# Performance work log

Hardware: AMD Instinct MI355X
Metric: run time of the kernel (lower is better)

Reference implementation:

```python
import jax, jax.numpy as jnp
import numpy as np

IN_DIM = 16384; DM = 512; DEPTH = 4
DI = 1024   # d_inner = expand * d_model
DS = 16     # d_state
DC = 4      # d_conv
DR = 32     # dt_rank = ceil(d_model/16)
B = 4; L = 256


def setup_inputs() -> dict:
    key = jax.random.key(0)
    ks = jax.random.split(key, 12)
    g = lambda k, s, sc=0.02: jax.random.normal(k, s, jnp.float32) * sc
    return {
        "x": jax.random.normal(ks[0], (B, L, IN_DIM), jnp.float32),
        # top-level projections / norm
        "in_w": g(ks[1], (DM, IN_DIM)), "in_b": jnp.zeros((DM,), jnp.float32),
        "ln_g": jnp.ones((DM,), jnp.float32), "ln_b": jnp.zeros((DM,), jnp.float32),
        "out_w": g(ks[2], (IN_DIM, DM)), "out_b": jnp.zeros((IN_DIM,), jnp.float32),
        # stacked per-layer Mamba params (leading dim = DEPTH)
        "m_in_w": g(ks[3], (DEPTH, 2 * DI, DM)),
        "conv_w": g(ks[4], (DEPTH, DI, DC), 0.2),
        "conv_b": jnp.zeros((DEPTH, DI), jnp.float32),
        "xproj_w": g(ks[5], (DEPTH, DR + 2 * DS, DI)),
        "dt_w": g(ks[6], (DEPTH, DI, DR), 0.1),
        "dt_b": jax.random.uniform(ks[7], (DEPTH, DI), jnp.float32, -4.0, -2.0),
        "A_log": jnp.log(jnp.broadcast_to(jnp.arange(1, DS + 1, dtype=jnp.float32), (DEPTH, DI, DS))),
        "D_p": jnp.ones((DEPTH, DI), jnp.float32),
        "m_out_w": g(ks[8], (DEPTH, DM, DI)),
    }


def _mamba(h, iw, cw, cb, xw, dw, db, Alog, Dp, ow):
    """One Mamba block (no residual, matching bare mamba_ssm.Mamba)."""
    Bn, Ln, _ = h.shape
    xz = h @ iw.T                                  # [B,L,2*DI]
    xc, z = jnp.split(xz, 2, axis=-1)
    # causal depthwise conv1d, kernel DC, truncated to L
    xp = jnp.pad(xc, ((0, 0), (DC - 1, 0), (0, 0)))
    conv = cb
    for k in range(DC):
        conv = conv + xp[:, k:k + Ln, :] * cw[:, k]
    xc = jax.nn.silu(conv)                         # [B,L,DI]
    xdbl = xc @ xw.T                               # [B,L,DR+2*DS]
    dt, Bm, Cm = xdbl[..., :DR], xdbl[..., DR:DR + DS], xdbl[..., DR + DS:]
    dt = jax.nn.softplus(dt @ dw.T + db)           # [B,L,DI]
    A = -jnp.exp(Alog)                             # [DI,DS]
    dA = jnp.exp(dt[..., None] * A)                # [B,L,DI,DS]
    dBx = dt[..., None] * Bm[:, :, None, :] * xc[..., None]  # [B,L,DI,DS]

    def step(hst, inp):
        a, b, c = inp
        hst = a * hst + b
        return hst, jnp.einsum('bdn,bn->bd', hst, c)

    h0 = jnp.zeros((Bn, DI, DS), xc.dtype)
    _, ys = jax.lax.scan(step, h0, (dA.transpose(1, 0, 2, 3), dBx.transpose(1, 0, 2, 3), Cm.transpose(1, 0, 2)))
    y = ys.transpose(1, 0, 2) + xc * Dp            # [B,L,DI]
    y = y * jax.nn.silu(z)
    return y @ ow.T                                # [B,L,DM]


def reference(x, in_w, in_b, ln_g, ln_b, out_w, out_b, m_in_w, conv_w, conv_b, xproj_w, dt_w, dt_b, A_log, D_p, m_out_w):
    h = x @ in_w.T + in_b                          # [B,L,DM]
    for i in range(DEPTH):
        h = _mamba(h, m_in_w[i], conv_w[i], conv_b[i], xproj_w[i], dt_w[i], dt_b[i], A_log[i], D_p[i], m_out_w[i])
    hl = h[:, -1]                                  # [B,DM]
    mu = hl.mean(-1, keepdims=True)
    var = ((hl - mu) ** 2).mean(-1, keepdims=True)
    hn = (hl - mu) / jnp.sqrt(var + 1e-5) * ln_g + ln_b
    return hn @ out_w.T + out_b                    # [B,IN_DIM]
```

## Files before the change

kernel.cpp:

```cpp
#include <hip/hip_runtime.h>
#include <stdint.h>

#define DEV static __device__ __forceinline__

typedef __attribute__((ext_vector_type(8))) __bf16 bf16x8;
typedef __attribute__((ext_vector_type(4))) float f32x4;

DEV float bfs2f(unsigned short u) {
    union { unsigned int i; float f; } c; c.i = ((unsigned int)u) << 16; return c.f;
}
DEV unsigned short f2bf(float v) {
    union { __bf16 b; unsigned short u; } c; c.b = (__bf16)v; return c.u;
}

template<int TH, int BM, int BN, int BK, int AMODE, int BMODE, int EPI, int CSPLIT>
__global__ __launch_bounds__(TH) void gemm_k(
    const void* __restrict__ A0, const void* __restrict__ A1,
    const void* __restrict__ B0, const void* __restrict__ B1,
    const float* __restrict__ bias,
    float* __restrict__ C0, float* __restrict__ C1,
    int lda, int ldb, int ldc, int Klen, int pstride)
{
    constexpr int NWN = TH / 128;
    constexpr int FM = BM / 2 / 16;
    constexpr int FN = BN / NWN / 16;
    constexpr int KB = BK / 32;
    constexpr int GAF = (AMODE == 0) ? BM * BK / (TH * 4) : 1;
    constexpr int GAP = (AMODE == 1) ? BM * BK / (TH * 8) : 1;
    constexpr int GBF = (BMODE == 0) ? BN * BK / (TH * 4) : 1;
    constexpr int GBP = (BMODE == 1) ? BN * BK / (TH * 8) : 1;

    __shared__ __align__(16) char smem[2 * (BM + BN) * BK * 2];
    char* sAh = smem;
    char* sAl = smem + BM * BK * 2;
    char* sBh = smem + 2 * BM * BK * 2;
    char* sBl = smem + 2 * BM * BK * 2 + BN * BK * 2;

    const int tid = threadIdx.x, lane = tid & 63;
    const int wid = tid >> 6;
    const int wm = wid & 1, wn = wid >> 1;
    const int q = lane >> 4, t16 = lane & 15;
    const int tileM = blockIdx.x * BM, tileN = blockIdx.y * BN;
    const int kBase = blockIdx.z * Klen, kEnd = kBase + Klen;
    float* C = C0 + (size_t)blockIdx.z * pstride;

    f32x4 acc[FM][FN];
#pragma unroll
    for (int a = 0; a < FM; ++a)
#pragma unroll
        for (int b = 0; b < FN; ++b) acc[a][b] = f32x4{0.f, 0.f, 0.f, 0.f};

    float4 aF[GAF], bF[GBF];
    int4 aH[GAP], aL[GAP], bH[GBP], bL[GBP];

    auto loadA = [&](int k0) {
        if (AMODE == 0) {
            const float* A32 = (const float*)A0;
#pragma unroll
            for (int u = 0; u < GAF; ++u) {
                int idx = u * TH + tid;
                int r = idx / (BK / 4), c4 = idx % (BK / 4);
                aF[u] = *(const float4*)(A32 + (size_t)(tileM + r) * lda + k0 + c4 * 4);
            }
        } else {
            const unsigned short* Ah = (const unsigned short*)A0;
            const unsigned short* Al = (const unsigned short*)A1;
#pragma unroll
            for (int u = 0; u < GAP; ++u) {
                int idx = u * TH + tid;
                int r = idx / (BK / 8), c8 = idx % (BK / 8);
                size_t src = (size_t)(tileM + r) * lda + k0 + c8 * 8;
                aH[u] = *(const int4*)(Ah + src);
                aL[u] = *(const int4*)(Al + src);
            }
        }
    };
    auto loadB = [&](int k0) {
        if (BMODE == 0) {
            const float* B32 = (const float*)B0;
#pragma unroll
            for (int u = 0; u < GBF; ++u) {
                int idx = u * TH + tid;
                int r = idx / (BK / 4), c4 = idx % (BK / 4);
                bF[u] = *(const float4*)(B32 + (size_t)(tileN + r) * ldb + k0 + c4 * 4);
            }
        } else {
            const unsigned short* Bh = (const unsigned short*)B0;
            const unsigned short* Bl = (const unsigned short*)B1;
#pragma unroll
            for (int u = 0; u < GBP; ++u) {
                int idx = u * TH + tid;
                int r = idx / (BK / 8), c8 = idx % (BK / 8);
                size_t src = (size_t)(tileN + r) * ldb + k0 + c8 * 8;
                bH[u] = *(const int4*)(Bh + src);
                bL[u] = *(const int4*)(Bl + src);
            }
        }
    };
    auto storeA = [&]() {
        if (AMODE == 0) {
#pragma unroll
            for (int u = 0; u < GAF; ++u) {
                int idx = u * TH + tid;
                int r = idx / (BK / 4), c4 = idx % (BK / 4);
                float vv[4] = {aF[u].x, aF[u].y, aF[u].z, aF[u].w};
                ushort4 hv, lv;
                unsigned short* hp = (unsigned short*)&hv;
                unsigned short* lp = (unsigned short*)&lv;
#pragma unroll
                for (int e = 0; e < 4; ++e) {
                    unsigned short hb = f2bf(vv[e]);
                    hp[e] = hb; lp[e] = f2bf(vv[e] - bfs2f(hb));
                }
                int off = (c4 / 8) * BM * 64 + r * 64 + (c4 & 7) * 8;
                *(ushort4*)(sAh + off) = hv;
                *(ushort4*)(sAl + off) = lv;
            }
        } else {
#pragma unroll
            for (int u = 0; u < GAP; ++u) {
                int idx = u * TH + tid;
                int r = idx / (BK / 8), c8 = idx % (BK / 8);
                int off = (c8 / 4) * BM * 64 + r * 64 + (c8 & 3) * 16;
                *(int4*)(sAh + off) = aH[u];
                *(int4*)(sAl + off) = aL[u];
            }
        }
    };
    auto storeB = [&]() {
        if (BMODE == 0) {
#pragma unroll
            for (int u = 0; u < GBF; ++u) {
                int idx = u * TH + tid;
                int r = idx / (BK / 4), c4 = idx % (BK / 4);
                float vv[4] = {bF[u].x, bF[u].y, bF[u].z, bF[u].w};
                ushort4 hv, lv;
                unsigned short* hp = (unsigned short*)&hv;
                unsigned short* lp = (unsigned short*)&lv;
#pragma unroll
                for (int e = 0; e < 4; ++e) {
                    unsigned short hb = f2bf(vv[e]);
                    hp[e] = hb; lp[e] = f2bf(vv[e] - bfs2f(hb));
                }
                int off = (c4 / 8) * BN * 64 + r * 64 + (c4 & 7) * 8;
                *(ushort4*)(sBh + off) = hv;
                *(ushort4*)(sBl + off) = lv;
            }
        } else {
#pragma unroll
            for (int u = 0; u < GBP; ++u) {
                int idx = u * TH + tid;
                int r = idx / (BK / 8), c8 = idx % (BK / 8);
                int off = (c8 / 4) * BN * 64 + r * 64 + (c8 & 3) * 16;
                *(int4*)(sBh + off) = bH[u];
                *(int4*)(sBl + off) = bL[u];
            }
        }
    };

    loadA(kBase); loadB(kBase);
    for (int k0 = kBase; k0 < kEnd; k0 += BK) {
        storeA(); storeB();
        __syncthreads();
        if (k0 + BK < kEnd) { loadA(k0 + BK); loadB(k0 + BK); }
#pragma unroll
        for (int kb = 0; kb < KB; ++kb) {
            bf16x8 ah[FM], al[FM], bh[FN], bl[FN];
#pragma unroll
            for (int fm = 0; fm < FM; ++fm) {
                int off = kb * BM * 64 + (wm * (BM / 2) + fm * 16 + t16) * 64 + q * 16;
                ah[fm] = *(const bf16x8*)(sAh + off);
                al[fm] = *(const bf16x8*)(sAl + off);
            }
#pragma unroll
            for (int fn = 0; fn < FN; ++fn) {
                int off = kb * BN * 64 + (wn * (BN / NWN) + fn * 16 + t16) * 64 + q * 16;
                bh[fn] = *(const bf16x8*)(sBh + off);
                bl[fn] = *(const bf16x8*)(sBl + off);
            }
#pragma unroll
            for (int fm = 0; fm < FM; ++fm)
#pragma unroll
                for (int fn = 0; fn < FN; ++fn) {
                    acc[fm][fn] = __builtin_amdgcn_mfma_f32_16x16x32_bf16(ah[fm], bh[fn], acc[fm][fn], 0, 0, 0);
                    acc[fm][fn] = __builtin_amdgcn_mfma_f32_16x16x32_bf16(al[fm], bh[fn], acc[fm][fn], 0, 0, 0);
                    acc[fm][fn] = __builtin_amdgcn_mfma_f32_16x16x32_bf16(ah[fm], bl[fn], acc[fm][fn], 0, 0, 0);
                }
        }
        __syncthreads();
    }

#pragma unroll
    for (int fm = 0; fm < FM; ++fm) {
        int row0 = tileM + wm * (BM / 2) + fm * 16 + q * 4;
#pragma unroll
        for (int fn = 0; fn < FN; ++fn) {
            int col = tileN + wn * (BN / NWN) + fn * 16 + t16;
            float* Cd = C; int cc2 = col;
            if (CSPLIT && col >= ldc) { Cd = C1; cc2 = col - ldc; }
            float bv = (EPI == 2) ? bias[col] : 0.f;
#pragma unroll
            for (int r = 0; r < 4; ++r) {
                float v = acc[fm][fn][r];
                if (EPI == 2) { v = fminf(v + bv, 60.f); v = log1pf(__expf(v)); }
                Cd[(size_t)(row0 + r) * ldc + cc2] = v;
            }
        }
    }
}

__global__ __launch_bounds__(256) void reduce_k(
    const float* __restrict__ part, int Z, int pstride, int n,
    const float* __restrict__ bias, int colmask,
    unsigned short* __restrict__ hi, unsigned short* __restrict__ lo,
    float* __restrict__ hlast, int colbits)
{
    int i = blockIdx.x * 256 + threadIdx.x;
    if (i >= n) return;
    float s = 0.f;
    for (int z = 0; z < Z; ++z) s += part[(size_t)z * pstride + i];
    if (bias) s += bias[i & colmask];
    unsigned short hb = f2bf(s);
    hi[i] = hb; lo[i] = f2bf(s - bfs2f(hb));
    if (hlast) {
        int row = i >> colbits;
        if ((row & 255) == 255)
            hlast[((row >> 8) << colbits) + (i & colmask)] = s;
    }
}

__global__ __launch_bounds__(256) void conv_silu_k(
    const float* __restrict__ xb, const float* __restrict__ cw,
    const float* __restrict__ cb, unsigned short* __restrict__ xch,
    unsigned short* __restrict__ xcl)
{
    int i  = blockIdx.x * 256 + threadIdx.x;
    int d  = i & 1023;
    int bl = i >> 10;
    int l  = bl & 255;
    float a = cb[d];
#pragma unroll
    for (int k = 0; k < 4; ++k) {
        int ls = l + k - 3;
        if (ls >= 0) a += xb[(size_t)(bl + k - 3) * 1024 + d] * cw[d * 4 + k];
    }
    float v = a / (1.f + __expf(-a));
    unsigned short hb = f2bf(v);
    xch[i] = hb; xcl[i] = f2bf(v - bfs2f(hb));
}

__global__ __launch_bounds__(256) void scan_k(
    const float* __restrict__ zb,
    const unsigned short* __restrict__ xch, const unsigned short* __restrict__ xcl,
    const unsigned short* __restrict__ xdh, const unsigned short* __restrict__ xdl,
    const float* __restrict__ dt, const float* __restrict__ Alog,
    const float* __restrict__ Dp,
    unsigned short* __restrict__ ygh, unsigned short* __restrict__ ygl)
{
    __shared__ float sdt[2048], sxc[2048], szz[2048], sbc[2048];
    int b   = blockIdx.x >> 5;
    int d0  = (blockIdx.x & 31) << 5;
    int ch  = threadIdx.x >> 3;
    int d   = d0 + ch;
    int sub = threadIdx.x & 7;
    int j0  = sub * 2;
    float An[2], hst[2] = {0.f, 0.f};
    An[0] = -__expf(Alog[d * 16 + j0]);
    An[1] = -__expf(Alog[d * 16 + j0 + 1]);
    float Dd  = Dp[d];
    int   bl0 = b * 256;

    for (int c = 0; c < 4; ++c) {
        __syncthreads();
#pragma unroll
        for (int it = 0; it < 8; ++it) {
            int j2 = it * 256 + threadIdx.x;
            int ll = j2 >> 5, dd = j2 & 31;
            size_t row = (size_t)(bl0 + c * 64 + ll);
            size_t gi  = row * 1024 + d0 + dd;
            sdt[j2] = dt[gi];
            sxc[j2] = bfs2f(xch[gi]) + bfs2f(xcl[gi]);
            szz[j2] = zb[gi];
            size_t bi = row * 64 + 32 + dd;
            sbc[j2] = bfs2f(xdh[bi]) + bfs2f(xdl[bi]);
        }
        __syncthreads();
#pragma unroll 4
        for (int li = 0; li < 64; ++li) {
            float dtv = sdt[li * 32 + ch];
            float xcv = sxc[li * 32 + ch];
            float c1  = dtv * xcv;
            float dA0 = __expf(dtv * An[0]);
            float dA1 = __expf(dtv * An[1]);
            float B0  = sbc[li * 32 + j0],      B1 = sbc[li * 32 + j0 + 1];
            float C0  = sbc[li * 32 + 16 + j0], C1 = sbc[li * 32 + 16 + j0 + 1];
            hst[0] = dA0 * hst[0] + c1 * B0;
            hst[1] = dA1 * hst[1] + c1 * B1;
            float y = hst[0] * C0 + hst[1] * C1;
            y += __shfl_xor(y, 1);
            y += __shfl_xor(y, 2);
            y += __shfl_xor(y, 4);
            if (sub == 0) {
                float zv = szz[li * 32 + ch];
                float sg = zv / (1.f + __expf(-zv));
                float v  = (y + xcv * Dd) * sg;
                unsigned short hb = f2bf(v);
                size_t o = (size_t)(bl0 + c * 64 + li) * 1024 + d;
                ygh[o] = hb; ygl[o] = f2bf(v - bfs2f(hb));
            }
        }
    }
}

__global__ __launch_bounds__(512) void ln_k(
    const float* __restrict__ hlast, const float* __restrict__ g,
    const float* __restrict__ bb, float* __restrict__ hn)
{
    __shared__ float red[16];
    int b = blockIdx.x, k = threadIdx.x;
    float x = hlast[b * 512 + k];
    float s = x, s2 = x * x;
#pragma unroll
    for (int m = 32; m; m >>= 1) { s += __shfl_xor(s, m, 64); s2 += __shfl_xor(s2, m, 64); }
    if ((k & 63) == 0) { red[k >> 6] = s; red[8 + (k >> 6)] = s2; }
    __syncthreads();
    float ts = 0.f, ts2 = 0.f;
#pragma unroll
    for (int j = 0; j < 8; ++j) { ts += red[j]; ts2 += red[8 + j]; }
    float mu   = ts * (1.f / 512.f);
    float var  = ts2 * (1.f / 512.f) - mu * mu;
    float rstd = rsqrtf(var + 1e-5f);
    hn[b * 512 + k] = (x - mu) * rstd * g[k] + bb[k];
}

__global__ __launch_bounds__(256) void final_k(
    const float* __restrict__ hn, const float* __restrict__ W,
    const float* __restrict__ ob, float* __restrict__ out)
{
    int wid = threadIdx.x >> 6, lane = threadIdx.x & 63;
    float a[4][8];
#pragma unroll
    for (int b2 = 0; b2 < 4; ++b2) {
        float4 v0 = *(const float4*)&hn[b2 * 512 + lane * 8];
        float4 v1 = *(const float4*)&hn[b2 * 512 + lane * 8 + 4];
        a[b2][0] = v0.x; a[b2][1] = v0.y; a[b2][2] = v0.z; a[b2][3] = v0.w;
        a[b2][4] = v1.x; a[b2][5] = v1.y; a[b2][6] = v1.z; a[b2][7] = v1.w;
    }
#pragma unroll 1
    for (int it = 0; it < 8; ++it) {
        int n = blockIdx.x * 4 + wid + it * 2048;
        const float* W32 = W + (size_t)n * 512 + lane * 8;
        float4 v0 = *(const float4*)W32;
        float4 v1 = *(const float4*)(W32 + 4);
        float wf[8] = {v0.x, v0.y, v0.z, v0.w, v1.x, v1.y, v1.z, v1.w};
        float s0 = 0.f, s1 = 0.f, s2 = 0.f, s3 = 0.f;
#pragma unroll
        for (int j = 0; j < 8; ++j) {
            s0 += a[0][j] * wf[j]; s1 += a[1][j] * wf[j];
            s2 += a[2][j] * wf[j]; s3 += a[3][j] * wf[j];
        }
#pragma unroll
        for (int m = 32; m; m >>= 1) {
            s0 += __shfl_xor(s0, m, 64); s1 += __shfl_xor(s1, m, 64);
            s2 += __shfl_xor(s2, m, 64); s3 += __shfl_xor(s3, m, 64);
        }
        if (lane == 0) {
            float bv = ob[n];
            out[0 * 16384 + n] = s0 + bv;
            out[1 * 16384 + n] = s1 + bv;
            out[2 * 16384 + n] = s2 + bv;
            out[3 * 16384 + n] = s3 + bv;
        }
    }
}

extern "C" void kernel_launch(void* const* d_in, const int* in_sizes, int n_in,
                              void* d_out, int out_size, void* d_ws, size_t ws_size,
                              hipStream_t stream)
{
    const float* x      = (const float*)d_in[0];
    const float* in_w   = (const float*)d_in[1];
    const float* in_b   = (const float*)d_in[2];
    const float* ln_g   = (const float*)d_in[3];
    const float* ln_b   = (const float*)d_in[4];
    const float* out_w  = (const float*)d_in[5];
    const float* out_b  = (const float*)d_in[6];
    const float* m_in_w = (const float*)d_in[7];
    const float* conv_w = (const float*)d_in[8];
    const float* conv_b = (const float*)d_in[9];
    const float* xproj_w= (const float*)d_in[10];
    const float* dt_w   = (const float*)d_in[11];
    const float* dt_b   = (const float*)d_in[12];
    const float* A_log  = (const float*)d_in[13];
    const float* D_p    = (const float*)d_in[14];
    const float* m_out_w= (const float*)d_in[15];

    char* W = (char*)d_ws;
    unsigned short* hplh = (unsigned short*)(W + 0);
    unsigned short* hpll = (unsigned short*)(W + 1048576);
    float* hlast = (float*)(W + 2097152);
    float* hn    = (float*)(W + 2162688);
    float* xbuf  = (float*)(W + 2228224);
    float* zbuf  = (float*)(W + 6422528);
    unsigned short* xch = (unsigned short*)(W + 10616832);
    unsigned short* xcl = (unsigned short*)(W + 12713984);
    float* dtb   = (float*)(W + 14811136);
    unsigned short* xdbh  = (unsigned short*)(W + 19005440);
    unsigned short* xdbl_ = (unsigned short*)(W + 19136512);
    float* part1 = (float*)(W + 2228224);
    float* partx = (float*)(W + 14811136);
    float* parto = (float*)(W + 6422528);
    unsigned short* ygh = (unsigned short*)(W + 2228224);
    unsigned short* ygl = (unsigned short*)(W + 4325376);

    gemm_k<512,128,128,64,0,0,0,0><<<dim3(8,4,8),512,0,stream>>>(
        x, nullptr, in_w, nullptr, nullptr, part1, nullptr,
        16384, 16384, 512, 2048, 524288);
    reduce_k<<<2048,256,0,stream>>>(part1, 8, 524288, 524288, in_b, 511,
                                    hplh, hpll, hlast, 9);

    for (int i = 0; i < 4; ++i) {
        const float* iw = m_in_w  + (size_t)i * 1048576;
        const float* cw = conv_w  + (size_t)i * 4096;
        const float* cb = conv_b  + (size_t)i * 1024;
        const float* xw = xproj_w + (size_t)i * 65536;
        const float* dw = dt_w    + (size_t)i * 32768;
        const float* db = dt_b    + (size_t)i * 1024;
        const float* Al = A_log   + (size_t)i * 16384;
        const float* Dp = D_p     + (size_t)i * 1024;
        const float* ow = m_out_w + (size_t)i * 524288;

        gemm_k<512,64,128,64,1,0,0,1><<<dim3(16,16,1),512,0,stream>>>(
            hplh, hpll, iw, nullptr, nullptr, xbuf, zbuf, 512, 512, 1024, 512, 0);
        conv_silu_k<<<4096,256,0,stream>>>(xbuf, cw, cb, xch, xcl);
        gemm_k<256,64,64,64,1,0,0,0><<<dim3(16,1,16),256,0,stream>>>(
            xch, xcl, xw, nullptr, nullptr, partx, nullptr, 1024, 1024, 64, 64, 65536);
        reduce_k<<<256,256,0,stream>>>(partx, 16, 65536, 65536, nullptr, 63,
                                       xdbh, xdbl_, nullptr, 6);
        gemm_k<256,64,64,32,1,0,2,0><<<dim3(16,16,1),256,0,stream>>>(
            xdbh, xdbl_, dw, nullptr, db, dtb, nullptr, 64, 32, 1024, 32, 0);
        scan_k<<<128,256,0,stream>>>(zbuf, xch, xcl, xdbh, xdbl_, dtb, Al, Dp,
                                     ygh, ygl);
        gemm_k<512,64,128,64,1,0,0,0><<<dim3(16,4,4),512,0,stream>>>(
            ygh, ygl, ow, nullptr, nullptr, parto, nullptr, 1024, 1024, 512, 256, 524288);
        reduce_k<<<2048,256,0,stream>>>(parto, 4, 524288, 524288, nullptr, 511,
                                        hplh, hpll, hlast, 9);
    }

    ln_k<<<4,512,0,stream>>>(hlast, ln_g, ln_b, hn);
    final_k<<<512,256,0,stream>>>(hn, out_w, out_b, (float*)d_out);
}
```

Before: 743.0 us.

## Fuse dt projection and softplus into scan kernel, one state per thread

Removes the separate dt GEMM launch and its dtb buffer. The scan kernel now computes dt = softplus(xdbl[:32]·dt_w + dt_b) itself, with each channel's dt_w row held in registers. The scan is also remapped so each thread owns one state element (16 threads per channel, 16 channels per block). That doubles the grid to 256 blocks and adds one more shuffle step to the reduction. The aim is to save a launch and the dt global write/read, and to raise parallelism in the latency-bound sequential scan, at the cost of extra per-element FMA work inside the scan prologue.

```diff
diff --git a/kernel.cpp b/kernel.cpp
--- a/kernel.cpp
+++ b/kernel.cpp
@@ -253,55 +253,83 @@
     const float* __restrict__ zb,
     const unsigned short* __restrict__ xch, const unsigned short* __restrict__ xcl,
     const unsigned short* __restrict__ xdh, const unsigned short* __restrict__ xdl,
-    const float* __restrict__ dt, const float* __restrict__ Alog,
-    const float* __restrict__ Dp,
+    const float* __restrict__ dw, const float* __restrict__ db,
+    const float* __restrict__ Alog, const float* __restrict__ Dp,
     unsigned short* __restrict__ ygh, unsigned short* __restrict__ ygl)
 {
-    __shared__ float sdt[2048], sxc[2048], szz[2048], sbc[2048];
-    int b   = blockIdx.x >> 5;
-    int d0  = (blockIdx.x & 31) << 5;
-    int ch  = threadIdx.x >> 3;
+    __shared__ float sdt[1024], sxc[1024], szz[1024], sbc[2048];
+    int b   = blockIdx.x >> 6;
+    int d0  = (blockIdx.x & 63) << 4;
+    int ch  = threadIdx.x >> 4;
     int d   = d0 + ch;
-    int sub = threadIdx.x & 7;
-    int j0  = sub * 2;
-    float An[2], hst[2] = {0.f, 0.f};
-    An[0] = -__expf(Alog[d * 16 + j0]);
-    An[1] = -__expf(Alog[d * 16 + j0 + 1]);
+    int sub = threadIdx.x & 15;
+    float An  = -__expf(Alog[d * 16 + sub]);
+    float hst = 0.f;
     float Dd  = Dp[d];
     int   bl0 = b * 256;
 
+    float dwreg[32];
+    {
+        const float4* p = (const float4*)(dw + (size_t)(d0 + sub) * 32);
+#pragma unroll
+        for (int w = 0; w < 8; ++w) {
+            float4 v = p[w];
+            dwreg[w * 4 + 0] = v.x; dwreg[w * 4 + 1] = v.y;
+            dwreg[w * 4 + 2] = v.z; dwreg[w * 4 + 3] = v.w;
+        }
+    }
+    float dbreg = db[d0 + sub];
+
     for (int c = 0; c < 4; ++c) {
         __syncthreads();
 #pragma unroll
+        for (int it = 0; it < 4; ++it) {
+            int j2 = it * 256 + threadIdx.x;
+            int ll = j2 >> 4;
+            size_t row = (size_t)(bl0 + c * 64 + ll);
+            size_t gi  = row * 1024 + d0 + sub;
+            sxc[j2] = bfs2f(xch[gi]) + bfs2f(xcl[gi]);
+            szz[j2] = zb[gi];
+            const int4* ph = (const int4*)(xdh + row * 64);
+            const int4* pl = (const int4*)(xdl + row * 64);
+            float s = dbreg;
+#pragma unroll
+            for (int w = 0; w < 4; ++w) {
+                int4 hv = ph[w], lv = pl[w];
+                const unsigned short* hp = (const unsigned short*)&hv;
+                const unsigned short* lp = (const unsigned short*)&lv;
+#pragma unroll
+                for (int e = 0; e < 8; ++e)
+                    s += (bfs2f(hp[e]) + bfs2f(lp[e])) * dwreg[w * 8 + e];
+            }
+            s = fminf(s, 60.f);
+            sdt[j2] = log1pf(__expf(s));
+        }
+#pragma unroll
         for (int it = 0; it < 8; ++it) {
             int j2 = it * 256 + threadIdx.x;
-            int ll = j2 >> 5, dd = j2 & 31;
+            int ll = j2 >> 5, nn = j2 & 31;
             size_t row = (size_t)(bl0 + c * 64 + ll);
-            size_t gi  = row * 1024 + d0 + dd;
-            sdt[j2] = dt[gi];
-            sxc[j2] = bfs2f(xch[gi]) + bfs2f(xcl[gi]);
-            szz[j2] = zb[gi];
-            size_t bi = row * 64 + 32 + dd;
+            size_t bi  = row * 64 + 32 + nn;
             sbc[j2] = bfs2f(xdh[bi]) + bfs2f(xdl[bi]);
         }
         __syncthreads();
 #pragma unroll 4
         for (int li = 0; li < 64; ++li) {
-            float dtv = sdt[li * 32 + ch];
-            float xcv = sxc[li * 32 + ch];
+            float dtv = sdt[li * 16 + ch];
+            float xcv = sxc[li * 16 + ch];
             float c1  = dtv * xcv;
-            float dA0 = __expf(dtv * An[0]);
-            float dA1 = __expf(dtv * An[1]);
-            float B0  = sbc[li * 32 + j0],      B1 = sbc[li * 32 + j0 + 1];
-            float C0  = sbc[li * 32 + 16 + j0], C1 = sbc[li * 32 + 16 + j0 + 1];
-            hst[0] = dA0 * hst[0] + c1 * B0;
-            hst[1] = dA1 * hst[1] + c1 * B1;
-            float y = hst[0] * C0 + hst[1] * C1;
+            float dA  = __expf(dtv * An);
+            float Bv  = sbc[li * 32 + sub];
+            float Cv  = sbc[li * 32 + 16 + sub];
+            hst = dA * hst + c1 * Bv;
+            float y = hst * Cv;
             y += __shfl_xor(y, 1);
             y += __shfl_xor(y, 2);
             y += __shfl_xor(y, 4);
+            y += __shfl_xor(y, 8);
             if (sub == 0) {
-                float zv = szz[li * 32 + ch];
+                float zv = szz[li * 16 + ch];
                 float sg = zv / (1.f + __expf(-zv));
                 float v  = (y + xcv * Dd) * sg;
                 unsigned short hb = f2bf(v);
@@ -404,7 +432,6 @@
     float* zbuf  = (float*)(W + 6422528);
     unsigned short* xch = (unsigned short*)(W + 10616832);
     unsigned short* xcl = (unsigned short*)(W + 12713984);
-    float* dtb   = (float*)(W + 14811136);
     unsigned short* xdbh  = (unsigned short*)(W + 19005440);
     unsigned short* xdbl_ = (unsigned short*)(W + 19136512);
     float* part1 = (float*)(W + 2228224);
@@ -437,10 +464,8 @@
             xch, xcl, xw, nullptr, nullptr, partx, nullptr, 1024, 1024, 64, 64, 65536);
         reduce_k<<<256,256,0,stream>>>(partx, 16, 65536, 65536, nullptr, 63,
                                        xdbh, xdbl_, nullptr, 6);
-        gemm_k<256,64,64,32,1,0,2,0><<<dim3(16,16,1),256,0,stream>>>(
-            xdbh, xdbl_, dw, nullptr, db, dtb, nullptr, 64, 32, 1024, 32, 0);
-        scan_k<<<128,256,0,stream>>>(zbuf, xch, xcl, xdbh, xdbl_, dtb, Al, Dp,
-                                     ygh, ygl);
+        scan_k<<<256,256,0,stream>>>(zbuf, xch, xcl, xdbh, xdbl_, dw, db,
+                                     Al, Dp, ygh, ygl);
         gemm_k<512,64,128,64,1,0,0,0><<<dim3(16,4,4),512,0,stream>>>(
             ygh, ygl, ow, nullptr, nullptr, parto, nullptr, 1024, 1024, 512, 256, 524288);
         reduce_k<<<2048,256,0,stream>>>(parto, 4, 524288, 524288, nullptr, 511,
```

Result: slower. 812.0 us (+9.3%).
